# Kernel optimization log

Measured on AMD Instinct MI355X. Metric: run time of the kernel, lower is better.

The kernel has to match this reference:

```python
import jax, jax.numpy as jnp
import numpy as np

B = 1024
IN_Q = 2048
IN_KV = 2048
NH = 16
D = 64
INNER = NH * D
TF = 4
NC = 2
EPS = 1e-5
SLOPE = 0.01  # LeakyReLU default negative slope


def setup_inputs() -> dict:
    key = jax.random.key(0)
    ks = jax.random.split(key, 8)
    s = 0.02
    return {
        "q_input": jax.random.normal(ks[0], (B, IN_Q), jnp.float32),
        "kv_input": jax.random.normal(ks[1], (B, IN_KV), jnp.float32),
        "Wq": jax.random.normal(ks[2], (INNER, IN_Q), jnp.float32) * s,
        "bq": jax.random.normal(ks[3], (INNER,), jnp.float32) * s,
        "Wkv": jax.random.normal(ks[4], (2 * INNER, IN_KV), jnp.float32) * s,
        "bkv": jax.random.normal(ks[5], (2 * INNER,), jnp.float32) * s,
        "bn_w": jnp.ones((TF,), jnp.float32),
        "bn_b": jnp.zeros((TF,), jnp.float32),
        "Wo": jax.random.normal(ks[6], (NC, TF), jnp.float32) * s,
        "bo": jax.random.normal(ks[7], (NC,), jnp.float32) * s,
    }


def reference(q_input, kv_input, Wq, bq, Wkv, bkv, bn_w, bn_b, Wo, bo):
    b = q_input.shape[0]
    # projections: [B, NH, D] and [B, NH, 2D]
    q = (q_input @ Wq.T + bq).reshape(b, NH, D)
    kv = (kv_input @ Wkv.T + bkv).reshape(b, NH, 2 * D)
    k, v = kv[..., :D], kv[..., D:]
    # sim[b,n] = k[b,n,:] . q[b,n,:]  (per-head scalar score)
    sim = jnp.einsum("bnd,bnd->bn", k, q)
    att = jax.nn.softmax(sim, axis=-1)  # softmax over heads
    # torch.matmul([B,NH], [B,NH,D]) broadcast -> out[i,j,:] = sum_n att[j,n] v[i,n,:]
    att_out = jnp.einsum("jn,ind->ijd", att, v)  # [B, B, D]
    flat = att_out.reshape(b, b * D)  # [B, B*D]
    # AdaptiveAvgPool1d to TF bins (L % TF == 0 -> exact reshape-mean)
    pooled = flat.reshape(b, TF, (b * D) // TF).mean(axis=-1)  # [B, TF]
    x = jnp.where(pooled >= 0, pooled, SLOPE * pooled)  # LeakyReLU
    # BatchNorm1d, train mode (batch stats, biased variance)
    mean = x.mean(axis=0)
    var = x.var(axis=0)
    x = (x - mean) * jax.lax.rsqrt(var + EPS) * bn_w + bn_b
    # dropout(p=0.0) is identity
    return x @ Wo.T + bo  # [B, NC]
```

## Files before the change

### kernel.cpp

```cpp
#include <hip/hip_runtime.h>
#include <hip/hip_bf16.h>

#define EPS 1e-5f
#define SLOPE 0.01f

typedef __attribute__((ext_vector_type(8))) short bfrag8;
typedef __attribute__((ext_vector_type(4))) float f32x4;

#define AS1 __attribute__((address_space(1)))
#define AS3 __attribute__((address_space(3)))

#define WS_SIM_OFF   0u
#define WS_S_OFF     65536u
#define WS_WVS_OFF   131072u
#define WS_BVS_OFF   262144u
#define WS_WBT_OFF   262208u

__device__ __forceinline__ unsigned short f2bf(float f) {
    union { float f; unsigned int u; } x; x.f = f;
    unsigned int r = (x.u + 0x7FFFu + ((x.u >> 16) & 1u)) >> 16;
    return (unsigned short)r;
}
__device__ __forceinline__ uint4 pack8(const float4& a, const float4& b) {
    uint4 r;
    r.x = (unsigned)f2bf(a.x) | ((unsigned)f2bf(a.y) << 16);
    r.y = (unsigned)f2bf(a.z) | ((unsigned)f2bf(a.w) << 16);
    r.z = (unsigned)f2bf(b.x) | ((unsigned)f2bf(b.y) << 16);
    r.w = (unsigned)f2bf(b.z) | ((unsigned)f2bf(b.w) << 16);
    return r;
}

#define PREP_B   524288
#define PREP_WVSE (PREP_B + 32768)
#define PREP_SIME (PREP_WVSE + 16384)
#define PREP_END  (PREP_SIME + 16)

__global__ __launch_bounds__(256) void prep_kernel(
        const float* __restrict__ Wq, const float* __restrict__ bq,
        const float* __restrict__ Wkv, const float* __restrict__ bkv,
        unsigned char* __restrict__ ws) {
    int gid = blockIdx.x * 256 + threadIdx.x;
    if (gid < PREP_B) {
        unsigned short* wbt = (unsigned short*)(ws + WS_WBT_OFF);
        int kkg = gid & 3;
        int col = (gid >> 2) & 127;
        int ks  = (gid >> 9) & 1;
        int it  = (gid >> 10) & 31;
        int h   = gid >> 15;
        const float* wrow = (col < 64) ? (Wq  + (size_t)(h * 64 + col) * 2048)
                                       : (Wkv + (size_t)(h * 128 + (col - 64)) * 2048);
        int k0 = it * 64 + ks * 32 + kkg * 8;
        float4 v0 = *(const float4*)(wrow + k0);
        float4 v1 = *(const float4*)(wrow + k0 + 4);
        *(uint4*)(wbt + (size_t)gid * 8) = pack8(v0, v1);
    } else if (gid < PREP_WVSE) {
        int g2 = gid - PREP_B;
        int n = g2 >> 11, c = g2 & 2047;
        const float* base = Wkv + (size_t)(n * 128 + 64) * 2048 + c;
        float s = 0.f;
        #pragma unroll 8
        for (int d = 0; d < 64; ++d) s += base[(size_t)d * 2048];
        ((float*)(ws + WS_WVS_OFF))[c * 16 + n] = s;
    } else if (gid < PREP_SIME) {
        ((float*)(ws + WS_SIM_OFF))[gid - PREP_WVSE] = 0.f;
    } else if (gid < PREP_END) {
        int n = gid - PREP_SIME;
        float b = 0.f;
        #pragma unroll
        for (int d = 0; d < 64; ++d) b += bkv[n * 128 + 64 + d];
        ((float*)(ws + WS_BVS_OFF))[n] = b;
    }
}

__global__ __launch_bounds__(512) void gemm_sim_kernel(
        const float* __restrict__ qin, const float* __restrict__ kvin,
        const float* __restrict__ bq, const float* __restrict__ bkv,
        unsigned char* __restrict__ ws) {
    __shared__ alignas(16) unsigned short Bt[4][2][128][32];
    __shared__ alignas(16) unsigned short At[2][2][2][64][32];
    __shared__ alignas(16) float Cqs[2][2][32][32];

    const int t = threadIdx.x;
    const int w = t >> 6, l = t & 63;
    const int h = blockIdx.x, mb = blockIdx.y;
    const int m0 = mb * 64;
    const int qk = w >> 2, rm = (w >> 1) & 1, dw = w & 1;
    const int lrow = l & 15, lko = (l >> 4) * 8;
    const int cb = qk * 64 + dw * 32;

    const unsigned char* wtile0 = ws + WS_WBT_OFF + (size_t)h * (32 * 16384);
    float* sim = (float*)(ws + WS_SIM_OFF);
    unsigned short* at0 = &At[0][0][0][0][0];
    unsigned short* bt0 = &Bt[0][0][0][0];

    f32x4 acc[2][2];
    acc[0][0] = (f32x4)0.f; acc[0][1] = (f32x4)0.f;
    acc[1][0] = (f32x4)0.f; acc[1][1] = (f32x4)0.f;

    const int aks = t >> 8, arow = (t >> 2) & 63, akkg = t & 3;
    const float* aq_src = qin  + (size_t)(m0 + arow) * 2048 + aks * 32 + akkg * 8;
    const float* ak_src = kvin + (size_t)(m0 + arow) * 2048 + aks * 32 + akkg * 8;
    const int awoff = aks * 2048 + arow * 32 + akkg * 8;

#define STAGE_B(ktile, buf) do {                                                   \
    const unsigned char* _src = wtile0 + (size_t)(ktile) * 16384;                  \
    unsigned char* _dst = ((unsigned char*)bt0) + (buf) * 16384;                   \
    _Pragma("unroll")                                                              \
    for (int _jj = 0; _jj < 2; ++_jj) {                                            \
        int _lin = _jj * 512 + t;                                                  \
        __builtin_amdgcn_global_load_lds(                                          \
            (const AS1 unsigned int*)(const void*)(_src + _lin * 16),              \
            (AS3 unsigned int*)(void*)(_dst + _lin * 16), 16, 0, 0);               \
    } } while (0)

#define LOAD_A(ktile, q0, q1, k0, k1) do {                                         \
    const float* _q = aq_src + (ktile) * 64;                                       \
    const float* _k = ak_src + (ktile) * 64;                                       \
    q0 = *(const float4*)_q;  q1 = *(const float4*)(_q + 4);                       \
    k0 = *(const float4*)_k;  k1 = *(const float4*)(_k + 4); } while (0)

#define WRITE_A(buf, q0, q1, k0, k1) do {                                          \
    *(uint4*)(at0 + (buf) * 8192 + awoff)        = pack8(q0, q1);                  \
    *(uint4*)(at0 + (buf) * 8192 + 4096 + awoff) = pack8(k0, k1); } while (0)

#define COMPUTE(abuf, bbuf) do {                                                   \
    const unsigned short* _Ab = at0 + (abuf) * 8192 + qk * 4096;                   \
    const unsigned short* _Bb = bt0 + (bbuf) * 8192;                               \
    _Pragma("unroll")                                                              \
    for (int _ks = 0; _ks < 2; ++_ks) {                                            \
        bfrag8 _fa0 = *(const bfrag8*)(_Ab + _ks * 2048 + (rm * 32 + lrow) * 32 + lko);      \
        bfrag8 _fa1 = *(const bfrag8*)(_Ab + _ks * 2048 + (rm * 32 + 16 + lrow) * 32 + lko); \
        bfrag8 _fb0 = *(const bfrag8*)(_Bb + _ks * 4096 + (cb + lrow) * 32 + lko);           \
        bfrag8 _fb1 = *(const bfrag8*)(_Bb + _ks * 4096 + (cb + 16 + lrow) * 32 + lko);      \
        acc[0][0] = __builtin_amdgcn_mfma_f32_16x16x32_bf16(_fa0, _fb0, acc[0][0], 0, 0, 0); \
        acc[0][1] = __builtin_amdgcn_mfma_f32_16x16x32_bf16(_fa0, _fb1, acc[0][1], 0, 0, 0); \
        acc[1][0] = __builtin_amdgcn_mfma_f32_16x16x32_bf16(_fa1, _fb0, acc[1][0], 0, 0, 0); \
        acc[1][1] = __builtin_amdgcn_mfma_f32_16x16x32_bf16(_fa1, _fb1, acc[1][1], 0, 0, 0); \
    } } while (0)

    float4 s0q0, s0q1, s0k0, s0k1;
    float4 s1q0, s1q1, s1k0, s1k1;

    STAGE_B(0, 0);
    STAGE_B(1, 1);
    LOAD_A(0, s0q0, s0q1, s0k0, s0k1);
    LOAD_A(1, s1q0, s1q1, s1k0, s1k1);
    WRITE_A(0, s0q0, s0q1, s0k0, s0k1);

    for (int ii = 0; ii < 8; ++ii) {
        #pragma unroll
        for (int u = 0; u < 4; ++u) {
            const int j = ii * 4 + u;
            if (j < 30) {
                STAGE_B(j + 2, (u + 2) & 3);
                if ((u & 1) == 0) LOAD_A(j + 2, s0q0, s0q1, s0k0, s0k1);
                else              LOAD_A(j + 2, s1q0, s1q1, s1k0, s1k1);
            }
            if (j < 31) {
                if ((u & 1) == 0) WRITE_A((u + 1) & 1, s1q0, s1q1, s1k0, s1k1);
                else              WRITE_A((u + 1) & 1, s0q0, s0q1, s0k0, s0k1);
            }
            if (j < 30) asm volatile("s_waitcnt vmcnt(6)" ::: "memory");
            else        asm volatile("s_waitcnt vmcnt(0)" ::: "memory");
            asm volatile("s_waitcnt lgkmcnt(0)" ::: "memory");
            __builtin_amdgcn_sched_barrier(0);
            __builtin_amdgcn_s_barrier();
            __builtin_amdgcn_sched_barrier(0);
            COMPUTE(u & 1, u & 3);
        }
    }

    float biasv[2];
    #pragma unroll
    for (int ni = 0; ni < 2; ++ni) {
        int d = dw * 32 + ni * 16 + lrow;
        biasv[ni] = qk ? bkv[h * 128 + d] : bq[h * 64 + d];
    }
    #pragma unroll
    for (int mi = 0; mi < 2; ++mi)
        #pragma unroll
        for (int ni = 0; ni < 2; ++ni)
            #pragma unroll
            for (int r = 0; r < 4; ++r)
                acc[mi][ni][r] += biasv[ni];

    if (!qk) {
        #pragma unroll
        for (int mi = 0; mi < 2; ++mi)
            #pragma unroll
            for (int ni = 0; ni < 2; ++ni)
                #pragma unroll
                for (int r = 0; r < 4; ++r)
                    Cqs[rm][dw][mi * 16 + (l >> 4) * 4 + r][ni * 16 + lrow] = acc[mi][ni][r];
    }
    __syncthreads();
    if (qk) {
        #pragma unroll
        for (int mi = 0; mi < 2; ++mi) {
            float p[4];
            #pragma unroll
            for (int r = 0; r < 4; ++r) {
                int r32 = mi * 16 + (l >> 4) * 4 + r;
                p[r] = Cqs[rm][dw][r32][lrow]      * acc[mi][0][r]
                     + Cqs[rm][dw][r32][16 + lrow] * acc[mi][1][r];
            }
            #pragma unroll
            for (int r = 0; r < 4; ++r) {
                float v = p[r];
                v += __shfl_xor(v, 1); v += __shfl_xor(v, 2);
                v += __shfl_xor(v, 4); v += __shfl_xor(v, 8);
                if ((l & 15) == 0) {
                    int row = m0 + rm * 32 + mi * 16 + (l >> 4) * 4 + r;
                    atomicAdd(&sim[row * 16 + h], v);
                }
            }
        }
    }
#undef STAGE_B
#undef LOAD_A
#undef WRITE_A
#undef COMPUTE
}

__global__ __launch_bounds__(256) void s_kernel(
        const float* __restrict__ kvin, unsigned char* __restrict__ ws) {
    int b = blockIdx.x, t = threadIdx.x;
    int w = t >> 6, l = t & 63;
    __shared__ float SW[4][16];
    int n = t & 15, g = t >> 4;
    const float* kvrow = kvin + (size_t)b * 2048;
    const float* wv = (const float*)(ws + WS_WVS_OFF);
    float p = 0.f;
    #pragma unroll 4
    for (int tt = 0; tt < 128; ++tt) {
        int c = g + (tt << 4);
        p = fmaf(kvrow[c], wv[c * 16 + n], p);
    }
    p += __shfl_xor(p, 16);
    p += __shfl_xor(p, 32);
    if (l < 16) SW[w][n] = p;
    __syncthreads();
    if (t < 16) {
        float sv = SW[0][t] + SW[1][t] + SW[2][t] + SW[3][t]
                 + ((const float*)(ws + WS_BVS_OFF))[t];
        ((float*)(ws + WS_S_OFF))[b * 16 + t] = sv;
    }
}

__global__ __launch_bounds__(1024) void final_kernel(
        const float* __restrict__ bn_w, const float* __restrict__ bn_b,
        const float* __restrict__ Wo, const float* __restrict__ bo,
        const unsigned char* __restrict__ ws, float* __restrict__ out) {
    int t = threadIdx.x;
    int w = t >> 6;
    int l = t & 63;
    __shared__ float Aw[16][16];
    __shared__ float Af[4][16];
    __shared__ float SWs[16][8];
    __shared__ float FS[8];
    __shared__ float sc[4], sh[4];

    float a16[16];
    {
        const float* srow = (const float*)(ws + WS_SIM_OFF) + (size_t)t * 16;
        float4 v0 = *(const float4*)(srow + 0);
        float4 v1 = *(const float4*)(srow + 4);
        float4 v2 = *(const float4*)(srow + 8);
        float4 v3 = *(const float4*)(srow + 12);
        a16[0]=v0.x; a16[1]=v0.y; a16[2]=v0.z; a16[3]=v0.w;
        a16[4]=v1.x; a16[5]=v1.y; a16[6]=v1.z; a16[7]=v1.w;
        a16[8]=v2.x; a16[9]=v2.y; a16[10]=v2.z; a16[11]=v2.w;
        a16[12]=v3.x; a16[13]=v3.y; a16[14]=v3.z; a16[15]=v3.w;
        float m = a16[0];
        #pragma unroll
        for (int n = 1; n < 16; ++n) m = fmaxf(m, a16[n]);
        float den = 0.f;
        #pragma unroll
        for (int n = 0; n < 16; ++n) { a16[n] = expf(a16[n] - m); den += a16[n]; }
        float inv = 1.f / den;
        #pragma unroll
        for (int n = 0; n < 16; ++n) a16[n] *= inv;
    }
    #pragma unroll
    for (int n = 0; n < 16; ++n) {
        float p = a16[n];
        p += __shfl_xor(p, 1);  p += __shfl_xor(p, 2);
        p += __shfl_xor(p, 4);  p += __shfl_xor(p, 8);
        p += __shfl_xor(p, 16); p += __shfl_xor(p, 32);
        a16[n] = p;
    }
    if (l == 0) {
        #pragma unroll
        for (int n = 0; n < 16; ++n) Aw[w][n] = a16[n];
    }
    __syncthreads();
    if (t < 64) {
        int f = t >> 4, n = t & 15;
        Af[f][n] = Aw[4*f][n] + Aw[4*f+1][n] + Aw[4*f+2][n] + Aw[4*f+3][n];
    }
    __syncthreads();

    float sv[16];
    {
        const float* srow = (const float*)(ws + WS_S_OFF) + (size_t)t * 16;
        float4 v0 = *(const float4*)(srow + 0);
        float4 v1 = *(const float4*)(srow + 4);
        float4 v2 = *(const float4*)(srow + 8);
        float4 v3 = *(const float4*)(srow + 12);
        sv[0]=v0.x; sv[1]=v0.y; sv[2]=v0.z; sv[3]=v0.w;
        sv[4]=v1.x; sv[5]=v1.y; sv[6]=v1.z; sv[7]=v1.w;
        sv[8]=v2.x; sv[9]=v2.y; sv[10]=v2.z; sv[11]=v2.w;
        sv[12]=v3.x; sv[13]=v3.y; sv[14]=v3.z; sv[15]=v3.w;
    }
    float x[4];
    #pragma unroll
    for (int f = 0; f < 4; ++f) {
        float p = 0.f;
        #pragma unroll
        for (int n = 0; n < 16; ++n) p = fmaf(Af[f][n], sv[n], p);
        p *= (1.f / 16384.f);
        x[f] = (p >= 0.f) ? p : SLOPE * p;
    }

    float st[8];
    #pragma unroll
    for (int f = 0; f < 4; ++f) { st[f] = x[f]; st[4 + f] = x[f] * x[f]; }
    #pragma unroll
    for (int j = 0; j < 8; ++j) {
        float p = st[j];
        p += __shfl_xor(p, 1);  p += __shfl_xor(p, 2);
        p += __shfl_xor(p, 4);  p += __shfl_xor(p, 8);
        p += __shfl_xor(p, 16); p += __shfl_xor(p, 32);
        st[j] = p;
    }
    if (l == 0) {
        #pragma unroll
        for (int j = 0; j < 8; ++j) SWs[w][j] = st[j];
    }
    __syncthreads();
    if (t < 8) {
        float p = 0.f;
        #pragma unroll
        for (int ww = 0; ww < 16; ++ww) p += SWs[ww][t];
        FS[t] = p;
    }
    __syncthreads();
    if (t < 4) {
        float mean = FS[t] * (1.f / 1024.f);
        float var  = FS[4 + t] * (1.f / 1024.f) - mean * mean;
        float s = bn_w[t] / sqrtf(var + EPS);
        sc[t] = s;
        sh[t] = bn_b[t] - mean * s;
    }
    __syncthreads();

    float o0 = bo[0], o1 = bo[1];
    #pragma unroll
    for (int f = 0; f < 4; ++f) {
        float xh = x[f] * sc[f] + sh[f];
        o0 = fmaf(xh, Wo[f], o0);
        o1 = fmaf(xh, Wo[4 + f], o1);
    }
    *(float2*)(out + (size_t)t * 2) = make_float2(o0, o1);
}

extern "C" void kernel_launch(void* const* d_in, const int* in_sizes, int n_in,
                              void* d_out, int out_size, void* d_ws, size_t ws_size,
                              hipStream_t stream) {
    const float* q_input  = (const float*)d_in[0];
    const float* kv_input = (const float*)d_in[1];
    const float* Wq   = (const float*)d_in[2];
    const float* bq   = (const float*)d_in[3];
    const float* Wkv  = (const float*)d_in[4];
    const float* bkv  = (const float*)d_in[5];
    const float* bn_w = (const float*)d_in[6];
    const float* bn_b = (const float*)d_in[7];
    const float* Wo   = (const float*)d_in[8];
    const float* bo   = (const float*)d_in[9];
    float* out = (float*)d_out;
    unsigned char* ws = (unsigned char*)d_ws;

    hipLaunchKernelGGL(prep_kernel, dim3((PREP_END + 255) / 256), dim3(256), 0, stream,
                       Wq, bq, Wkv, bkv, ws);
    hipLaunchKernelGGL(gemm_sim_kernel, dim3(16, 16), dim3(512), 0, stream,
                       q_input, kv_input, bq, bkv, ws);
    hipLaunchKernelGGL(s_kernel, dim3(1024), dim3(256), 0, stream, kv_input, ws);
    hipLaunchKernelGGL(final_kernel, dim3(1), dim3(1024), 0, stream,
                       bn_w, bn_b, Wo, bo, ws, out);
}
```

Measured before the change: 67.63 us.

## Pre-swizzle A and B into MFMA fragment layout and drop LDS staging

The prep kernel now also converts the q and kv activations to bf16 and writes both activations and weights in per-lane MFMA fragment order. The GEMM then loads fragments straight from global memory into registers through a three-deep register pipeline, with no shared-memory staging and no barriers. This removes LDS traffic and synchronisation from the main loop. In exchange it adds an extra global write and read of the converted activations, and each A fragment is now read again by all 16 head blocks instead of being shared through LDS.

```diff
diff --git a/kernel.cpp b/kernel.cpp
--- a/kernel.cpp
+++ b/kernel.cpp
@@ -6,15 +6,13 @@
 
 typedef __attribute__((ext_vector_type(8))) short bfrag8;
 typedef __attribute__((ext_vector_type(4))) float f32x4;
-
-#define AS1 __attribute__((address_space(1)))
-#define AS3 __attribute__((address_space(3)))
 
 #define WS_SIM_OFF   0u
 #define WS_S_OFF     65536u
 #define WS_WVS_OFF   131072u
 #define WS_BVS_OFF   262144u
-#define WS_WBT_OFF   262208u
+#define WS_AIMG_OFF  262208u
+#define WS_BIMG_OFF  8650816u
 
 __device__ __forceinline__ unsigned short f2bf(float f) {
     union { float f; unsigned int u; } x; x.f = f;
@@ -30,31 +28,49 @@
     return r;
 }
 
-#define PREP_B   524288
-#define PREP_WVSE (PREP_B + 32768)
+#define PREP_A   524288
+#define PREP_B2  (PREP_A + 524288)
+#define PREP_WVSE (PREP_B2 + 32768)
 #define PREP_SIME (PREP_WVSE + 16384)
 #define PREP_END  (PREP_SIME + 16)
 
 __global__ __launch_bounds__(256) void prep_kernel(
-        const float* __restrict__ Wq, const float* __restrict__ bq,
-        const float* __restrict__ Wkv, const float* __restrict__ bkv,
-        unsigned char* __restrict__ ws) {
+        const float* __restrict__ qin, const float* __restrict__ kvin,
+        const float* __restrict__ Wq, const float* __restrict__ Wkv,
+        const float* __restrict__ bkv, unsigned char* __restrict__ ws) {
     int gid = blockIdx.x * 256 + threadIdx.x;
-    if (gid < PREP_B) {
-        unsigned short* wbt = (unsigned short*)(ws + WS_WBT_OFF);
-        int kkg = gid & 3;
-        int col = (gid >> 2) & 127;
-        int ks  = (gid >> 9) & 1;
-        int it  = (gid >> 10) & 31;
-        int h   = gid >> 15;
-        const float* wrow = (col < 64) ? (Wq  + (size_t)(h * 64 + col) * 2048)
-                                       : (Wkv + (size_t)(h * 128 + (col - 64)) * 2048);
-        int k0 = it * 64 + ks * 32 + kkg * 8;
+    if (gid < PREP_A) {
+        int l  = gid & 63;
+        int mi = (gid >> 6) & 1;
+        int ks = (gid >> 7) & 1;
+        int kt = (gid >> 8) & 31;
+        int rm = (gid >> 13) & 1;
+        int mbb = (gid >> 14) & 15;
+        int qq = gid >> 18;
+        int row = mbb * 64 + rm * 32 + mi * 16 + (l & 15);
+        int k0  = kt * 64 + ks * 32 + (l >> 4) * 8;
+        const float* src = (qq ? kvin : qin) + (size_t)row * 2048 + k0;
+        float4 v0 = *(const float4*)src;
+        float4 v1 = *(const float4*)(src + 4);
+        *(uint4*)(ws + WS_AIMG_OFF + (size_t)gid * 16) = pack8(v0, v1);
+    } else if (gid < PREP_B2) {
+        int g2 = gid - PREP_A;
+        int l  = g2 & 63;
+        int ni = (g2 >> 6) & 1;
+        int ks = (g2 >> 7) & 1;
+        int kt = (g2 >> 8) & 31;
+        int dww = (g2 >> 13) & 1;
+        int qq  = (g2 >> 14) & 1;
+        int hh  = g2 >> 15;
+        int col = qq * 64 + dww * 32 + ni * 16 + (l & 15);
+        int k0  = kt * 64 + ks * 32 + (l >> 4) * 8;
+        const float* wrow = (col < 64) ? (Wq  + (size_t)(hh * 64 + col) * 2048)
+                                       : (Wkv + (size_t)(hh * 128 + (col - 64)) * 2048);
         float4 v0 = *(const float4*)(wrow + k0);
         float4 v1 = *(const float4*)(wrow + k0 + 4);
-        *(uint4*)(wbt + (size_t)gid * 8) = pack8(v0, v1);
+        *(uint4*)(ws + WS_BIMG_OFF + (size_t)g2 * 16) = pack8(v0, v1);
     } else if (gid < PREP_WVSE) {
-        int g2 = gid - PREP_B;
+        int g2 = gid - PREP_B2;
         int n = g2 >> 11, c = g2 & 2047;
         const float* base = Wkv + (size_t)(n * 128 + 64) * 2048 + c;
         float s = 0.f;
@@ -73,11 +89,8 @@
 }
 
 __global__ __launch_bounds__(512) void gemm_sim_kernel(
-        const float* __restrict__ qin, const float* __restrict__ kvin,
         const float* __restrict__ bq, const float* __restrict__ bkv,
         unsigned char* __restrict__ ws) {
-    __shared__ alignas(16) unsigned short Bt[4][2][128][32];
-    __shared__ alignas(16) unsigned short At[2][2][2][64][32];
     __shared__ alignas(16) float Cqs[2][2][32][32];
 
     const int t = threadIdx.x;
@@ -85,90 +98,53 @@
     const int h = blockIdx.x, mb = blockIdx.y;
     const int m0 = mb * 64;
     const int qk = w >> 2, rm = (w >> 1) & 1, dw = w & 1;
-    const int lrow = l & 15, lko = (l >> 4) * 8;
-    const int cb = qk * 64 + dw * 32;
-
-    const unsigned char* wtile0 = ws + WS_WBT_OFF + (size_t)h * (32 * 16384);
+    const int lrow = l & 15;
+
+    const unsigned char* aP = ws + WS_AIMG_OFF
+        + (size_t)(((qk * 16 + mb) * 2 + rm) * 32) * 4096 + l * 16;
+    const unsigned char* bP = ws + WS_BIMG_OFF
+        + (size_t)(((h * 2 + qk) * 2 + dw) * 32) * 4096 + l * 16;
     float* sim = (float*)(ws + WS_SIM_OFF);
-    unsigned short* at0 = &At[0][0][0][0][0];
-    unsigned short* bt0 = &Bt[0][0][0][0];
-
-    f32x4 acc[2][2];
-    acc[0][0] = (f32x4)0.f; acc[0][1] = (f32x4)0.f;
-    acc[1][0] = (f32x4)0.f; acc[1][1] = (f32x4)0.f;
-
-    const int aks = t >> 8, arow = (t >> 2) & 63, akkg = t & 3;
-    const float* aq_src = qin  + (size_t)(m0 + arow) * 2048 + aks * 32 + akkg * 8;
-    const float* ak_src = kvin + (size_t)(m0 + arow) * 2048 + aks * 32 + akkg * 8;
-    const int awoff = aks * 2048 + arow * 32 + akkg * 8;
-
-#define STAGE_B(ktile, buf) do {                                                   \
-    const unsigned char* _src = wtile0 + (size_t)(ktile) * 16384;                  \
-    unsigned char* _dst = ((unsigned char*)bt0) + (buf) * 16384;                   \
-    _Pragma("unroll")                                                              \
-    for (int _jj = 0; _jj < 2; ++_jj) {                                            \
-        int _lin = _jj * 512 + t;                                                  \
-        __builtin_amdgcn_global_load_lds(                                          \
-            (const AS1 unsigned int*)(const void*)(_src + _lin * 16),              \
-            (AS3 unsigned int*)(void*)(_dst + _lin * 16), 16, 0, 0);               \
-    } } while (0)
-
-#define LOAD_A(ktile, q0, q1, k0, k1) do {                                         \
-    const float* _q = aq_src + (ktile) * 64;                                       \
-    const float* _k = ak_src + (ktile) * 64;                                       \
-    q0 = *(const float4*)_q;  q1 = *(const float4*)(_q + 4);                       \
-    k0 = *(const float4*)_k;  k1 = *(const float4*)(_k + 4); } while (0)
-
-#define WRITE_A(buf, q0, q1, k0, k1) do {                                          \
-    *(uint4*)(at0 + (buf) * 8192 + awoff)        = pack8(q0, q1);                  \
-    *(uint4*)(at0 + (buf) * 8192 + 4096 + awoff) = pack8(k0, k1); } while (0)
-
-#define COMPUTE(abuf, bbuf) do {                                                   \
-    const unsigned short* _Ab = at0 + (abuf) * 8192 + qk * 4096;                   \
-    const unsigned short* _Bb = bt0 + (bbuf) * 8192;                               \
-    _Pragma("unroll")                                                              \
-    for (int _ks = 0; _ks < 2; ++_ks) {                                            \
-        bfrag8 _fa0 = *(const bfrag8*)(_Ab + _ks * 2048 + (rm * 32 + lrow) * 32 + lko);      \
-        bfrag8 _fa1 = *(const bfrag8*)(_Ab + _ks * 2048 + (rm * 32 + 16 + lrow) * 32 + lko); \
-        bfrag8 _fb0 = *(const bfrag8*)(_Bb + _ks * 4096 + (cb + lrow) * 32 + lko);           \
-        bfrag8 _fb1 = *(const bfrag8*)(_Bb + _ks * 4096 + (cb + 16 + lrow) * 32 + lko);      \
-        acc[0][0] = __builtin_amdgcn_mfma_f32_16x16x32_bf16(_fa0, _fb0, acc[0][0], 0, 0, 0); \
-        acc[0][1] = __builtin_amdgcn_mfma_f32_16x16x32_bf16(_fa0, _fb1, acc[0][1], 0, 0, 0); \
-        acc[1][0] = __builtin_amdgcn_mfma_f32_16x16x32_bf16(_fa1, _fb0, acc[1][0], 0, 0, 0); \
-        acc[1][1] = __builtin_amdgcn_mfma_f32_16x16x32_bf16(_fa1, _fb1, acc[1][1], 0, 0, 0); \
-    } } while (0)
-
-    float4 s0q0, s0q1, s0k0, s0k1;
-    float4 s1q0, s1q1, s1k0, s1k1;
-
-    STAGE_B(0, 0);
-    STAGE_B(1, 1);
-    LOAD_A(0, s0q0, s0q1, s0k0, s0k1);
-    LOAD_A(1, s1q0, s1q1, s1k0, s1k1);
-    WRITE_A(0, s0q0, s0q1, s0k0, s0k1);
-
-    for (int ii = 0; ii < 8; ++ii) {
-        #pragma unroll
-        for (int u = 0; u < 4; ++u) {
-            const int j = ii * 4 + u;
-            if (j < 30) {
-                STAGE_B(j + 2, (u + 2) & 3);
-                if ((u & 1) == 0) LOAD_A(j + 2, s0q0, s0q1, s0k0, s0k1);
-                else              LOAD_A(j + 2, s1q0, s1q1, s1k0, s1k1);
-            }
-            if (j < 31) {
-                if ((u & 1) == 0) WRITE_A((u + 1) & 1, s1q0, s1q1, s1k0, s1k1);
-                else              WRITE_A((u + 1) & 1, s0q0, s0q1, s0k0, s0k1);
-            }
-            if (j < 30) asm volatile("s_waitcnt vmcnt(6)" ::: "memory");
-            else        asm volatile("s_waitcnt vmcnt(0)" ::: "memory");
-            asm volatile("s_waitcnt lgkmcnt(0)" ::: "memory");
-            __builtin_amdgcn_sched_barrier(0);
-            __builtin_amdgcn_s_barrier();
-            __builtin_amdgcn_sched_barrier(0);
-            COMPUTE(u & 1, u & 3);
-        }
-    }
+
+    f32x4 acc00 = (f32x4)0.f, acc01 = (f32x4)0.f, acc10 = (f32x4)0.f, acc11 = (f32x4)0.f;
+
+#define DECL_SET(S) bfrag8 S##a00, S##a01, S##a10, S##a11, S##b00, S##b01, S##b10, S##b11
+#define LOADS(kt, S) do {                                                     \
+    const unsigned char* _a = aP + (size_t)(kt) * 4096;                       \
+    const unsigned char* _b = bP + (size_t)(kt) * 4096;                       \
+    S##a00 = *(const bfrag8*)(_a);                                            \
+    S##a01 = *(const bfrag8*)(_a + 1024);                                     \
+    S##a10 = *(const bfrag8*)(_a + 2048);                                     \
+    S##a11 = *(const bfrag8*)(_a + 3072);                                     \
+    S##b00 = *(const bfrag8*)(_b);                                            \
+    S##b01 = *(const bfrag8*)(_b + 1024);                                     \
+    S##b10 = *(const bfrag8*)(_b + 2048);                                     \
+    S##b11 = *(const bfrag8*)(_b + 3072);                                     \
+} while (0)
+#define COMP(S) do {                                                                        \
+    acc00 = __builtin_amdgcn_mfma_f32_16x16x32_bf16(S##a00, S##b00, acc00, 0, 0, 0);        \
+    acc01 = __builtin_amdgcn_mfma_f32_16x16x32_bf16(S##a00, S##b01, acc01, 0, 0, 0);        \
+    acc10 = __builtin_amdgcn_mfma_f32_16x16x32_bf16(S##a01, S##b00, acc10, 0, 0, 0);        \
+    acc11 = __builtin_amdgcn_mfma_f32_16x16x32_bf16(S##a01, S##b01, acc11, 0, 0, 0);        \
+    acc00 = __builtin_amdgcn_mfma_f32_16x16x32_bf16(S##a10, S##b10, acc00, 0, 0, 0);        \
+    acc01 = __builtin_amdgcn_mfma_f32_16x16x32_bf16(S##a10, S##b11, acc01, 0, 0, 0);        \
+    acc10 = __builtin_amdgcn_mfma_f32_16x16x32_bf16(S##a11, S##b10, acc10, 0, 0, 0);        \
+    acc11 = __builtin_amdgcn_mfma_f32_16x16x32_bf16(S##a11, S##b11, acc11, 0, 0, 0);        \
+} while (0)
+
+    DECL_SET(P0_); DECL_SET(P1_); DECL_SET(P2_);
+    LOADS(0, P0_);
+    LOADS(1, P1_);
+    for (int kt = 0; kt < 30; kt += 3) {
+        LOADS(kt + 2, P2_);  COMP(P0_);
+        LOADS(kt + 3, P0_);  COMP(P1_);
+        LOADS(kt + 4, P1_);  COMP(P2_);
+    }
+    COMP(P0_);
+    COMP(P1_);
+#undef DECL_SET
+#undef LOADS
+#undef COMP
 
     float biasv[2];
     #pragma unroll
@@ -176,6 +152,7 @@
         int d = dw * 32 + ni * 16 + lrow;
         biasv[ni] = qk ? bkv[h * 128 + d] : bq[h * 64 + d];
     }
+    f32x4 acc[2][2] = {{acc00, acc01}, {acc10, acc11}};
     #pragma unroll
     for (int mi = 0; mi < 2; ++mi)
         #pragma unroll
@@ -216,10 +193,6 @@
             }
         }
     }
-#undef STAGE_B
-#undef LOAD_A
-#undef WRITE_A
-#undef COMPUTE
 }
 
 __global__ __launch_bounds__(256) void s_kernel(
@@ -381,9 +354,9 @@
     unsigned char* ws = (unsigned char*)d_ws;
 
     hipLaunchKernelGGL(prep_kernel, dim3((PREP_END + 255) / 256), dim3(256), 0, stream,
-                       Wq, bq, Wkv, bkv, ws);
+                       q_input, kv_input, Wq, Wkv, bkv, ws);
     hipLaunchKernelGGL(gemm_sim_kernel, dim3(16, 16), dim3(512), 0, stream,
-                       q_input, kv_input, bq, bkv, ws);
+                       bq, bkv, ws);
     hipLaunchKernelGGL(s_kernel, dim3(1024), dim3(256), 0, stream, kv_input, ws);
     hipLaunchKernelGGL(final_kernel, dim3(1), dim3(1024), 0, stream,
                        bn_w, bn_b, Wo, bo, ws, out);
```

Result: no change. 66.59 us (-1.5%).
